# Optimization experiments

Hardware: AMD Instinct MI355X
Metric: run time of the kernel (lower is better)

The kernel has to match this reference:

```python
import jax, jax.numpy as jnp
import numpy as np

B, L, DIM, NH = 32, 512, 256, 4
HD = DIM // NH  # head_size = 64
SCALE = float(np.sqrt(HD))


def setup_inputs() -> dict:
    key = jax.random.key(0)
    k1, k2, k3, k4 = jax.random.split(key, 4)
    x = jax.random.normal(k1, (B, L, DIM), dtype=jnp.float32)
    adj = jax.random.randint(k2, (B, L, L), 0, 16, dtype=jnp.int32)
    w_qkv = jax.random.normal(k3, (3 * DIM, DIM), dtype=jnp.float32) * 0.02
    w_proj = jax.random.normal(k4, (DIM, DIM), dtype=jnp.float32) * 0.02
    return {"x": x, "adj": adj, "w_qkv": w_qkv, "w_proj": w_proj}


def reference(x, adj, w_qkv, w_proj):
    # qkv projection (torch Linear, no bias: y = x @ W.T)
    qkv = x @ w_qkv.T  # [B, L, 3*DIM]
    q, k, v = jnp.split(qkv, 3, axis=-1)
    q = q.reshape(B, L, NH, HD).transpose(0, 2, 1, 3)  # [B, H, L, HD]
    k = k.reshape(B, L, NH, HD).transpose(0, 2, 1, 3)
    v = v.reshape(B, L, NH, HD).transpose(0, 2, 1, 3)

    score = jnp.einsum('bhqd,bhkd->bhqk', q, k) / SCALE  # [B, H, L, L]

    # rel_pos_bias adjacency mask construction
    a = jnp.where((adj > 1) & (adj < 9), 0, adj)
    a = (a != 0).astype(jnp.float32)               # binarized adjacency [B, L, L]
    aT = jnp.swapaxes(a, -1, -2)
    pe = jnp.stack([a, aT, aT @ a, a @ aT], axis=1)  # [B, 4, L, L]
    pe = pe + jnp.eye(L, dtype=jnp.float32)
    pe = pe.astype(jnp.int32)

    score = jnp.where(pe == 0, -jnp.inf, score)
    attn = jax.nn.softmax(score, axis=-1)
    out = jnp.einsum('bhqk,bhkd->bhqd', attn, v)   # [B, H, L, HD]
    out = out.transpose(0, 2, 1, 3).reshape(B, L, DIM)
    return out @ w_proj.T
```

## Files before the change

### kernel.cpp

```cpp
#include <hip/hip_runtime.h>


typedef unsigned long long u64;
typedef unsigned short u16;
typedef short bf16x8 __attribute__((ext_vector_type(8)));
typedef float f32x4 __attribute__((ext_vector_type(4)));

#define MFMA16(a, b, c) __builtin_amdgcn_mfma_f32_16x16x32_bf16((a), (b), (c), 0, 0, 0)

__device__ __forceinline__ unsigned f2bf(float f) {
  unsigned u = __float_as_uint(f);
  return (u + 0x7FFFu + ((u >> 16) & 1u)) >> 16;
}
__device__ __forceinline__ float bf2f(unsigned b) { return __uint_as_float(b << 16); }

__device__ __forceinline__ unsigned cvtpk(float lo, float hi) {
  unsigned r;
  asm("v_cvt_pk_bf16_f32 %0, %1, %2" : "=v"(r) : "v"(lo), "v"(hi));
  return r;
}

__device__ __forceinline__ void gload16(const u16* src, u16* ldsDst) {
  __builtin_amdgcn_global_load_lds(
      (const __attribute__((address_space(1))) void*)src,
      (__attribute__((address_space(3))) void*)ldsDst, 16, 0, 0);
}

__device__ __forceinline__ int swzE(int row, int e) {
  return row * 64 + (e ^ ((row & 7) << 3));
}
__device__ __forceinline__ int swzV(int row, int c) {
  return row * 512 + (c ^ ((row & 7) << 3));
}

#define OFF_XB    ((size_t)0)
#define OFF_WQKV  ((size_t)8388608)
#define OFF_WPA   ((size_t)8781824)
#define OFF_QB    ((size_t)9175040)
#define OFF_KB    ((size_t)17563648)
#define OFF_VTB   ((size_t)25952256)
#define OFF_CTXA  ((size_t)34340864)
#define OFF_ROWR  ((size_t)51118080)
#define OFF_COLR  ((size_t)52166656)
#define OFF_MASK  ((size_t)53215232)

__global__ __launch_bounds__(512) void prep(const float* __restrict__ x, u16* __restrict__ xb,
                                            const float* __restrict__ wqkv, u16* __restrict__ wqkvb,
                                            const float* __restrict__ wp, u16* __restrict__ wpa,
                                            const int* __restrict__ adj, u64* __restrict__ rowraw,
                                            u64* __restrict__ maskA0) {
  int blk = blockIdx.x;
  if (blk < 1072) {
    const float* src = (blk < 1024) ? x : wqkv;
    u16* dst = (blk < 1024) ? xb : wqkvb;
    int bb = (blk < 1024) ? blk : (blk - 1024);
    size_t i = ((size_t)bb * 512 + threadIdx.x) * 8;
    float4 a = *(const float4*)(src + i);
    float4 c = *(const float4*)(src + i + 4);
    uint4 o;
    o.x = f2bf(a.x) | (f2bf(a.y) << 16);
    o.y = f2bf(a.z) | (f2bf(a.w) << 16);
    o.z = f2bf(c.x) | (f2bf(c.y) << 16);
    o.w = f2bf(c.z) | (f2bf(c.w) << 16);
    *(uint4*)(dst + i) = o;
  } else if (blk < 1200) {
    int idx = (blk - 1072) * 512 + threadIdx.x;
    int n = idx >> 8, k = idx & 255;
    float v = wp[idx];
    unsigned hi = f2bf(v);
    unsigned lo = f2bf(v - bf2f(hi));
    size_t base = (size_t)n * 768;
    wpa[base + k]       = (u16)hi;
    wpa[base + 256 + k] = (u16)hi;
    wpa[base + 512 + k] = (u16)lo;
  } else {
    int blk2 = blk - 1200;
    int b = blk2 >> 6, r0 = (blk2 & 63) * 8;
    int wave = threadIdx.x >> 6, lane = threadIdx.x & 63;
    #pragma unroll
    for (int rr = 0; rr < 8; ++rr) {
      int row = r0 + rr;
      int v = adj[((size_t)b * 512 + row) * 512 + wave * 64 + lane];
      u64 bal = __ballot(v == 1 || v >= 9);
      if (lane == 0) {
        size_t o = ((size_t)b * 512 + row) * 8 + wave;
        rowraw[o] = bal;
        maskA0[o] = bal | (((row >> 6) == wave) ? (1ull << (row & 63)) : 0ull);
      }
    }
  }
}

__global__ __launch_bounds__(512) void maskall(const u64* __restrict__ rowraw,
                                               u64* __restrict__ maskA1,
                                               u64* __restrict__ maskA2,
                                               u64* __restrict__ maskA3) {
  __shared__ u64 btr[8 * 512];
  __shared__ u64 cbuf[512 * 8];
  int b = blockIdx.x, tid = threadIdx.x;
  {
    const u64* src = rowraw + (size_t)b * 4096 + (size_t)tid * 8;
    u64 r[8];
    #pragma unroll
    for (int w = 0; w < 8; ++w) r[w] = src[w];
    #pragma unroll
    for (int w = 0; w < 8; ++w) btr[w * 512 + tid] = r[w];
  }
  __syncthreads();
  int w = tid >> 6, lane = tid & 63;
  u64 words[8];
  #pragma unroll
  for (int wd = 0; wd < 8; ++wd) {
    u64 word = btr[w * 512 + wd * 64 + lane];
    u64 mine = 0;
    #pragma unroll 1
    for (int c = 0; c < 64; ++c) {
      u64 bal = __ballot((word >> c) & 1ull);
      if (lane == c) mine = bal;
    }
    words[wd] = mine;
  }
  {
    u64* m1 = maskA1 + (size_t)b * 4096 + (size_t)tid * 8;
    #pragma unroll
    for (int wd = 0; wd < 8; ++wd) cbuf[tid * 8 + wd] = words[wd];
    words[w] |= (1ull << lane);
    #pragma unroll
    for (int wd = 0; wd < 8; ++wd) m1[wd] = words[wd];
  }
  __syncthreads();

  u64 myrow[8], mycol[8];
  #pragma unroll
  for (int w2 = 0; w2 < 8; ++w2) { myrow[w2] = btr[w2 * 512 + tid]; mycol[w2] = cbuf[tid * 8 + w2]; }
  u64 a2[8] = {0, 0, 0, 0, 0, 0, 0, 0}, a3[8] = {0, 0, 0, 0, 0, 0, 0, 0};
  for (int c0 = 0; c0 < 512; c0 += 64) {
    for (int cc = 0; cc < 64; ++cc) {
      int c = c0 + cc;
      u64 p3 = 0ull - ((myrow[c >> 6] >> (c & 63)) & 1ull);
      u64 p2 = 0ull - ((mycol[c >> 6] >> (c & 63)) & 1ull);
      #pragma unroll
      for (int w2 = 0; w2 < 8; ++w2) {
        a3[w2] |= cbuf[c * 8 + w2] & p3;
        a2[w2] |= btr[w2 * 512 + c] & p2;
      }
    }
    u64 f = ~0ull;
    #pragma unroll
    for (int w2 = 0; w2 < 8; ++w2) f &= (a2[w2] & a3[w2]);
    if (__all((int)(f == ~0ull))) break;
  }
  #pragma unroll
  for (int w2 = 0; w2 < 8; ++w2) {
    u64 eye = ((tid >> 6) == w2) ? (1ull << (tid & 63)) : 0ull;
    size_t o = (size_t)b * 4096 + (size_t)tid * 8 + w2;
    maskA2[o] = a2[w2] | eye;
    maskA3[o] = a3[w2] | eye;
  }
}

__global__ __launch_bounds__(256) void gemm_qkv(const u16* __restrict__ A,
                                                const u16* __restrict__ Bw,
                                                u16* __restrict__ o_q, u16* __restrict__ o_k,
                                                u16* __restrict__ o_v) {
  __shared__ u16 As[128 * 64];
  __shared__ u16 Bs[128 * 64];
  const int lin = blockIdx.x;
  const int logical = (lin & 7) * 96 + (lin >> 3);
  const int m0 = (logical / 6) * 128, n0 = (logical % 6) * 128;
  const int tid = threadIdx.x;
  const int lane = tid & 63, wid = tid >> 6;
  const int lg = lane >> 4, lc = lane & 15;
  const int wm = wid >> 1, wn = wid & 1;
  f32x4 acc[4][4] = {};

  const int srow = lane >> 3;
  const int schunk = ((lane & 7) ^ srow) * 8;
  #define STAGE_QKV(ks)                                                        \
    {                                                                          \
      int kk0 = (ks) * 64;                                                     \
      _Pragma("unroll")                                                        \
      for (int j = 0; j < 4; ++j) {                                            \
        int slab = wid * 4 + j;                                                \
        int r = slab * 8 + srow;                                               \
        gload16(A + (size_t)(m0 + r) * 256 + kk0 + schunk, &As[slab * 512]);   \
        gload16(Bw + (size_t)(n0 + r) * 256 + kk0 + schunk, &Bs[slab * 512]);  \
      }                                                                        \
    }

  STAGE_QKV(0);
  for (int ks = 0; ks < 4; ++ks) {
    __syncthreads();
    bf16x8 af[2][4], bf[2][4];
    #pragma unroll
    for (int kk = 0; kk < 2; ++kk)
      #pragma unroll
      for (int mi = 0; mi < 4; ++mi) {
        af[kk][mi] = *(const bf16x8*)&As[swzE(wm * 64 + mi * 16 + lc, kk * 32 + lg * 8)];
        bf[kk][mi] = *(const bf16x8*)&Bs[swzE(wn * 64 + mi * 16 + lc, kk * 32 + lg * 8)];
      }
    __syncthreads();
    if (ks < 3) STAGE_QKV(ks + 1);
    #pragma unroll
    for (int kk = 0; kk < 2; ++kk)
      #pragma unroll
      for (int mi = 0; mi < 4; ++mi)
        #pragma unroll
        for (int ni = 0; ni < 4; ++ni)
          acc[mi][ni] = MFMA16(af[kk][mi], bf[kk][ni], acc[mi][ni]);
  }
  #undef STAGE_QKV

  #pragma unroll
  for (int mi = 0; mi < 4; ++mi) {
    int mbase = m0 + wm * 64 + mi * 16 + lg * 4;
    int bb = mbase >> 9, l = mbase & 511;
    #pragma unroll
    for (int ni = 0; ni < 4; ++ni) {
      int n = n0 + wn * 64 + ni * 16 + lc;
      if (n < 512) {
        u16* dst = (n < 256) ? o_q : o_k;
        int c = n & 255, hh = c >> 6, dd = c & 63;
        size_t base = (((size_t)bb * 4 + hh) * 512 + l) * 64 + dd;
        #pragma unroll
        for (int r = 0; r < 4; ++r) dst[base + (size_t)r * 64] = (u16)f2bf(acc[mi][ni][r]);
      } else {
        int c = n - 512, hh = c >> 6, dd = c & 63;
        ushort4 pk;
        pk.x = (u16)f2bf(acc[mi][ni][0]); pk.y = (u16)f2bf(acc[mi][ni][1]);
        pk.z = (u16)f2bf(acc[mi][ni][2]); pk.w = (u16)f2bf(acc[mi][ni][3]);
        *(ushort4*)&o_v[(((size_t)bb * 4 + hh) * 64 + dd) * 512 + l] = pk;
      }
    }
  }
}

__global__ __launch_bounds__(256) void gemm_out(const u16* __restrict__ A,
                                                const u16* __restrict__ Bw,
                                                float* __restrict__ o_f) {
  __shared__ u16 As[64 * 64];
  __shared__ u16 Bs[128 * 64];
  const int lin = blockIdx.x;
  const int logical = (lin & 7) * 64 + (lin >> 3);
  const int m0 = (logical >> 1) * 64, n0 = (logical & 1) * 128;
  const int tid = threadIdx.x;
  const int lane = tid & 63, wid = tid >> 6;
  const int lg = lane >> 4, lc = lane & 15;
  const int wm = wid >> 1, wn = wid & 1;
  f32x4 acc[2][4] = {};

  const int srow = lane >> 3;
  const int schunk = ((lane & 7) ^ srow) * 8;
  #define STAGE_OUT(ks)                                                        \
    {                                                                          \
      int k0 = (ks) * 64;                                                      \
      int ka0 = (k0 >= 512) ? k0 - 512 : k0;                                   \
      _Pragma("unroll")                                                        \
      for (int j = 0; j < 2; ++j) {                                            \
        int slab = wid * 2 + j;                                                \
        int r = slab * 8 + srow;                                               \
        gload16(A + (size_t)(m0 + r) * 512 + ka0 + schunk, &As[slab * 512]);   \
      }                                                                        \
      _Pragma("unroll")                                                        \
      for (int j = 0; j < 4; ++j) {                                            \
        int slab = wid * 4 + j;                                                \
        int r = slab * 8 + srow;                                               \
        gload16(Bw + (size_t)(n0 + r) * 768 + k0 + schunk, &Bs[slab * 512]);   \
      }                                                                        \
    }

  STAGE_OUT(0);
  for (int ks = 0; ks < 12; ++ks) {
    __syncthreads();
    bf16x8 af[2][2], bf[2][4];
    #pragma unroll
    for (int kk = 0; kk < 2; ++kk) {
      #pragma unroll
      for (int mi = 0; mi < 2; ++mi)
        af[kk][mi] = *(const bf16x8*)&As[swzE(wm * 32 + mi * 16 + lc, kk * 32 + lg * 8)];
      #pragma unroll
      for (int ni = 0; ni < 4; ++ni)
        bf[kk][ni] = *(const bf16x8*)&Bs[swzE(wn * 64 + ni * 16 + lc, kk * 32 + lg * 8)];
    }
    __syncthreads();
    if (ks < 11) STAGE_OUT(ks + 1);
    #pragma unroll
    for (int kk = 0; kk < 2; ++kk)
      #pragma unroll
      for (int mi = 0; mi < 2; ++mi)
        #pragma unroll
        for (int ni = 0; ni < 4; ++ni)
          acc[mi][ni] = MFMA16(af[kk][mi], bf[kk][ni], acc[mi][ni]);
  }
  #undef STAGE_OUT

  #pragma unroll
  for (int mi = 0; mi < 2; ++mi) {
    int mbase = m0 + wm * 32 + mi * 16 + lg * 4;
    #pragma unroll
    for (int ni = 0; ni < 4; ++ni) {
      int n = n0 + wn * 64 + ni * 16 + lc;
      #pragma unroll
      for (int r = 0; r < 4; ++r) o_f[(size_t)(mbase + r) * 256 + n] = acc[mi][ni][r];
    }
  }
}

__device__ __forceinline__ void p_step(const f32x4 sT[4], u64 mw, int lane, u16* PsW,
                                       float& lrun, bf16x8& ap0, bf16x8& ap1) {
  const float SC = 0.125f * 1.4426950408889634f;
  const int lg = lane >> 4, lc = lane & 15;
  float p[4][4];
  float ps = 0.f;
  #pragma unroll
  for (int nf = 0; nf < 4; ++nf)
    #pragma unroll
    for (int r = 0; r < 4; ++r) {
      bool ok = (mw >> (nf * 16 + r)) & 1ull;
      float e = __builtin_amdgcn_exp2f(sT[nf][r] * SC);
      e = ok ? e : 0.f;
      p[nf][r] = e;
      ps += e;
    }
  lrun += ps;

  #pragma unroll
  for (int nf = 0; nf < 4; ++nf) {
    uint2 w2;
    w2.x = cvtpk(p[nf][0], p[nf][1]);
    w2.y = cvtpk(p[nf][2], p[nf][3]);
    *(uint2*)&PsW[swzE(lc, nf * 16 + lg * 4)] = w2;
  }
  ap0 = *(const bf16x8*)&PsW[swzE(lc, lg * 8)];
  ap1 = *(const bf16x8*)&PsW[swzE(lc, lg * 8 + 32)];
}

__global__ __launch_bounds__(512, 1) void attn(const u16* __restrict__ qb, const u16* __restrict__ kb,
                                               const u16* __restrict__ vtb, const u64* __restrict__ maskA,
                                               u16* __restrict__ ctxa) {
  __shared__ u16 Ks[512 * 64];
  __shared__ u16 Vs[64 * 512];
  __shared__ u16 Ps[8][16 * 64];
  const int lin = blockIdx.x;
  const int logical = (lin & 7) * 32 + (lin >> 3);
  const int bh = logical >> 1, half = logical & 1;
  const int b = bh >> 2, h = bh & 3;
  const int tid = threadIdx.x, lane = tid & 63, wid = tid >> 6;
  const int lg = lane >> 4, lc = lane & 15;

  {
    const u16* kgs = kb + (size_t)bh * 512 * 64;
    const u16* vgs = vtb + (size_t)bh * 64 * 512;
    const int srow = lane >> 3;
    const int schunk = ((lane & 7) ^ srow) * 8;
    #pragma unroll
    for (int j = 0; j < 8; ++j) {
      int slab = wid * 8 + j;
      gload16(kgs + (size_t)(slab * 8 + srow) * 64 + schunk, &Ks[slab * 512]);
    }
    #pragma unroll
    for (int j = 0; j < 8; ++j) {
      int vr = wid * 8 + j;
      gload16(vgs + (size_t)vr * 512 + ((lane ^ (vr & 7)) * 8), &Vs[vr * 512]);
    }
  }

  const int qrow0 = half * 256 + wid * 32;
  const u16* qgA = qb + ((size_t)bh * 512 + qrow0 + lc) * 64;
  const u16* qgB = qgA + 16 * 64;
  bf16x8 qA0 = *(const bf16x8*)(qgA + lg * 8);
  bf16x8 qA1 = *(const bf16x8*)(qgA + 32 + lg * 8);
  bf16x8 qB0 = *(const bf16x8*)(qgB + lg * 8);
  bf16x8 qB1 = *(const bf16x8*)(qgB + 32 + lg * 8);

  float lrunA = 0.f, lrunB = 0.f;
  f32x4 accoA[4] = {}, accoB[4] = {};
  const u64* mrowA = maskA + ((size_t)(h * 32 + b) * 512 + qrow0 + lc) * 8;
  const u64* mrowB = mrowA + 16 * 8;
  u16* PsW = Ps[wid];

  u64 mwA = mrowA[0], mwB = mrowB[0];

  __syncthreads();

  for (int kt = 0; kt < 8; ++kt) {
    u64 nmwA = (kt < 7) ? mrowA[kt + 1] : 0ull;
    u64 nmwB = (kt < 7) ? mrowB[kt + 1] : 0ull;

    f32x4 sA[4], sB[4];
    __builtin_amdgcn_s_setprio(1);
    #pragma unroll
    for (int nf = 0; nf < 4; ++nf) {
      bf16x8 ak0 = *(const bf16x8*)&Ks[swzE(kt * 64 + nf * 16 + lc, lg * 8)];
      bf16x8 ak1 = *(const bf16x8*)&Ks[swzE(kt * 64 + nf * 16 + lc, lg * 8 + 32)];
      f32x4 zA = {0.f, 0.f, 0.f, 0.f};
      zA = MFMA16(ak0, qA0, zA);
      zA = MFMA16(ak1, qA1, zA);
      sA[nf] = zA;
      f32x4 zB = {0.f, 0.f, 0.f, 0.f};
      zB = MFMA16(ak0, qB0, zB);
      zB = MFMA16(ak1, qB1, zB);
      sB[nf] = zB;
    }
    __builtin_amdgcn_s_setprio(0);

    bf16x8 apA0, apA1, apB0, apB1;
    p_step(sA, mwA >> (lg * 4), lane, PsW, lrunA, apA0, apA1);
    p_step(sB, mwB >> (lg * 4), lane, PsW, lrunB, apB0, apB1);

    __builtin_amdgcn_s_setprio(1);
    #pragma unroll
    for (int df = 0; df < 4; ++df) {
      bf16x8 bv0 = *(const bf16x8*)&Vs[swzV(df * 16 + lc, kt * 64 + lg * 8)];
      bf16x8 bv1 = *(const bf16x8*)&Vs[swzV(df * 16 + lc, kt * 64 + 32 + lg * 8)];
      accoA[df] = MFMA16(apA0, bv0, accoA[df]);
      accoA[df] = MFMA16(apA1, bv1, accoA[df]);
      accoB[df] = MFMA16(apB0, bv0, accoB[df]);
      accoB[df] = MFMA16(apB1, bv1, accoB[df]);
    }
    __builtin_amdgcn_s_setprio(0);

    mwA = nmwA;
    mwB = nmwB;
  }

  lrunA += __shfl_xor(lrunA, 16);
  lrunA += __shfl_xor(lrunA, 32);
  lrunB += __shfl_xor(lrunB, 16);
  lrunB += __shfl_xor(lrunB, 32);
  float lrA[4], lrB[4];
  #pragma unroll
  for (int r = 0; r < 4; ++r) {
    lrA[r] = 1.0f / __shfl(lrunA, (lane & 48) | (lg * 4 + r));
    lrB[r] = 1.0f / __shfl(lrunB, (lane & 48) | (lg * 4 + r));
  }
  #pragma unroll
  for (int r = 0; r < 4; ++r) {
    int rowq = qrow0 + lg * 4 + r;
    size_t baseA = ((size_t)b * 512 + rowq) * 512;
    size_t baseB = ((size_t)b * 512 + rowq + 16) * 512;
    #pragma unroll
    for (int df = 0; df < 4; ++df) {
      int c = h * 64 + df * 16 + lc;
      float vA = accoA[df][r] * lrA[r];
      unsigned hiA = f2bf(vA);
      ctxa[baseA + c]       = (u16)hiA;
      ctxa[baseA + 256 + c] = (u16)f2bf(vA - bf2f(hiA));
      float vB = accoB[df][r] * lrB[r];
      unsigned hiB = f2bf(vB);
      ctxa[baseB + c]       = (u16)hiB;
      ctxa[baseB + 256 + c] = (u16)f2bf(vB - bf2f(hiB));
    }
  }
}

extern "C" void kernel_launch(void* const* d_in, const int* in_sizes, int n_in,
                              void* d_out, int out_size, void* d_ws, size_t ws_size,
                              hipStream_t stream) {
  const float* x     = (const float*)d_in[0];
  const int*   adj   = (const int*)d_in[1];
  const float* wqkv  = (const float*)d_in[2];
  const float* wproj = (const float*)d_in[3];
  char* ws = (char*)d_ws;
  u16* xb     = (u16*)(ws + OFF_XB);
  u16* wqkvb  = (u16*)(ws + OFF_WQKV);
  u16* wpa    = (u16*)(ws + OFF_WPA);
  u16* qb     = (u16*)(ws + OFF_QB);
  u16* kb     = (u16*)(ws + OFF_KB);
  u16* vtb    = (u16*)(ws + OFF_VTB);
  u16* ctxa   = (u16*)(ws + OFF_CTXA);
  u64* rowraw = (u64*)(ws + OFF_ROWR);
  u64* maskA  = (u64*)(ws + OFF_MASK);
  const size_t MSTRIDE = (size_t)32 * 512 * 8;

  prep<<<dim3(3248), 512, 0, stream>>>(x, xb, wqkv, wqkvb, wproj, wpa, adj, rowraw, maskA);
  maskall<<<dim3(32), 512, 0, stream>>>(rowraw, maskA + MSTRIDE, maskA + 2 * MSTRIDE, maskA + 3 * MSTRIDE);
  gemm_qkv<<<dim3(768), 256, 0, stream>>>(xb, wqkvb, qb, kb, vtb);
  attn<<<dim3(256), 512, 0, stream>>>(qb, kb, vtb, maskA, ctxa);
  gemm_out<<<dim3(512), 256, 0, stream>>>(ctxa, wpa, (float*)d_out);
}
```

Baseline: 104.5 us.

## Split mask kernel into bit transpose and parallel mask products across more blocks

```diff
diff --git a/kernel.cpp b/kernel.cpp
--- a/kernel.cpp
+++ b/kernel.cpp
@@ -91,12 +91,10 @@
   }
 }
 
-__global__ __launch_bounds__(512) void maskall(const u64* __restrict__ rowraw,
-                                               u64* __restrict__ maskA1,
-                                               u64* __restrict__ maskA2,
-                                               u64* __restrict__ maskA3) {
+__global__ __launch_bounds__(512) void transpose_bits(const u64* __restrict__ rowraw,
+                                                      u64* __restrict__ colraw,
+                                                      u64* __restrict__ maskA1) {
   __shared__ u64 btr[8 * 512];
-  __shared__ u64 cbuf[512 * 8];
   int b = blockIdx.x, tid = threadIdx.x;
   {
     const u64* src = rowraw + (size_t)b * 4096 + (size_t)tid * 8;
@@ -120,43 +118,60 @@
     }
     words[wd] = mine;
   }
-  {
-    u64* m1 = maskA1 + (size_t)b * 4096 + (size_t)tid * 8;
-    #pragma unroll
-    for (int wd = 0; wd < 8; ++wd) cbuf[tid * 8 + wd] = words[wd];
-    words[w] |= (1ull << lane);
-    #pragma unroll
-    for (int wd = 0; wd < 8; ++wd) m1[wd] = words[wd];
+  int col = w * 64 + lane;
+  u64* crow = colraw + (size_t)b * 4096 + (size_t)col * 8;
+  u64* mrow = maskA1 + (size_t)b * 4096 + (size_t)col * 8;
+  #pragma unroll
+  for (int wd = 0; wd < 8; ++wd) crow[wd] = words[wd];
+  words[w] |= (1ull << lane);
+  #pragma unroll
+  for (int wd = 0; wd < 8; ++wd) mrow[wd] = words[wd];
+}
+
+__global__ __launch_bounds__(512) void mask23p(const u64* __restrict__ rowraw,
+                                               const u64* __restrict__ colraw,
+                                               u64* __restrict__ maskA2,
+                                               u64* __restrict__ maskA3) {
+  __shared__ u64 rb[4104];
+  __shared__ u64 cb[4104];
+  const int b = blockIdx.x, qc = blockIdx.y, tid = threadIdx.x;
+  for (int i = tid; i < 4096; i += 512) {
+    int li = i + (i >> 9);
+    rb[li] = rowraw[(size_t)b * 4096 + i];
+    cb[li] = colraw[(size_t)b * 4096 + i];
   }
   __syncthreads();
 
-  u64 myrow[8], mycol[8];
-  #pragma unroll
-  for (int w2 = 0; w2 < 8; ++w2) { myrow[w2] = btr[w2 * 512 + tid]; mycol[w2] = cbuf[tid * 8 + w2]; }
+  const int ql = tid >> 3, wg = tid & 7;
+  const int q = qc * 64 + ql;
+  const u64 myrow_w = rb[q * 8 + wg + (q >> 6)];
+  const u64 mycol_w = cb[q * 8 + wg + (q >> 6)];
+
   u64 a2[8] = {0, 0, 0, 0, 0, 0, 0, 0}, a3[8] = {0, 0, 0, 0, 0, 0, 0, 0};
-  for (int c0 = 0; c0 < 512; c0 += 64) {
-    for (int cc = 0; cc < 64; ++cc) {
-      int c = c0 + cc;
-      u64 p3 = 0ull - ((myrow[c >> 6] >> (c & 63)) & 1ull);
-      u64 p2 = 0ull - ((mycol[c >> 6] >> (c & 63)) & 1ull);
-      #pragma unroll
-      for (int w2 = 0; w2 < 8; ++w2) {
-        a3[w2] |= cbuf[c * 8 + w2] & p3;
-        a2[w2] |= btr[w2 * 512 + c] & p2;
-      }
-    }
-    u64 f = ~0ull;
-    #pragma unroll
-    for (int w2 = 0; w2 < 8; ++w2) f &= (a2[w2] & a3[w2]);
-    if (__all((int)(f == ~0ull))) break;
-  }
-  #pragma unroll
-  for (int w2 = 0; w2 < 8; ++w2) {
-    u64 eye = ((tid >> 6) == w2) ? (1ull << (tid & 63)) : 0ull;
-    size_t o = (size_t)b * 4096 + (size_t)tid * 8 + w2;
-    maskA2[o] = a2[w2] | eye;
-    maskA3[o] = a3[w2] | eye;
-  }
+  #pragma unroll 4
+  for (int cc = 0; cc < 64; ++cc) {
+    int base = (wg * 64 + cc) * 8 + wg;
+    u64 p3 = 0ull - ((myrow_w >> cc) & 1ull);
+    u64 p2 = 0ull - ((mycol_w >> cc) & 1ull);
+    #pragma unroll
+    for (int w = 0; w < 8; ++w) {
+      a3[w] |= cb[base + w] & p3;
+      a2[w] |= rb[base + w] & p2;
+    }
+  }
+
+  #pragma unroll
+  for (int off = 1; off < 8; off <<= 1)
+    #pragma unroll
+    for (int w = 0; w < 8; ++w) {
+      a2[w] |= __shfl_xor(a2[w], off);
+      a3[w] |= __shfl_xor(a3[w], off);
+    }
+
+  u64 eye = ((q >> 6) == wg) ? (1ull << (q & 63)) : 0ull;
+  size_t o = (size_t)b * 4096 + (size_t)q * 8 + wg;
+  maskA2[o] = a2[wg] | eye;
+  maskA3[o] = a3[wg] | eye;
 }
 
 __global__ __launch_bounds__(256) void gemm_qkv(const u16* __restrict__ A,
@@ -470,11 +485,13 @@
   u16* vtb    = (u16*)(ws + OFF_VTB);
   u16* ctxa   = (u16*)(ws + OFF_CTXA);
   u64* rowraw = (u64*)(ws + OFF_ROWR);
+  u64* colraw = (u64*)(ws + OFF_COLR);
   u64* maskA  = (u64*)(ws + OFF_MASK);
   const size_t MSTRIDE = (size_t)32 * 512 * 8;
 
   prep<<<dim3(3248), 512, 0, stream>>>(x, xb, wqkv, wqkvb, wproj, wpa, adj, rowraw, maskA);
-  maskall<<<dim3(32), 512, 0, stream>>>(rowraw, maskA + MSTRIDE, maskA + 2 * MSTRIDE, maskA + 3 * MSTRIDE);
+  transpose_bits<<<dim3(32), 512, 0, stream>>>(rowraw, colraw, maskA + MSTRIDE);
+  mask23p<<<dim3(32, 8), 512, 0, stream>>>(rowraw, colraw, maskA + 2 * MSTRIDE, maskA + 3 * MSTRIDE);
   gemm_qkv<<<dim3(768), 256, 0, stream>>>(xb, wqkvb, qb, kb, vtb);
   attn<<<dim3(256), 512, 0, stream>>>(qb, kb, vtb, maskA, ctxa);
   gemm_out<<<dim3(512), 256, 0, stream>>>(ctxa, wpa, (float*)d_out);
```

Result: slower. 114.3 us (+9.4%).

## Split boolean mask product into parallel transpose and per-word intersection kernels

Applied to the files above, without the earlier changes.

```diff
diff --git a/kernel.cpp b/kernel.cpp
--- a/kernel.cpp
+++ b/kernel.cpp
@@ -91,71 +91,54 @@
   }
 }
 
-__global__ __launch_bounds__(512) void maskall(const u64* __restrict__ rowraw,
-                                               u64* __restrict__ maskA1,
-                                               u64* __restrict__ maskA2,
-                                               u64* __restrict__ maskA3) {
-  __shared__ u64 btr[8 * 512];
-  __shared__ u64 cbuf[512 * 8];
-  int b = blockIdx.x, tid = threadIdx.x;
+__global__ __launch_bounds__(512) void transposeW(const u64* __restrict__ rowraw,
+                                                  u64* __restrict__ colraw,
+                                                  u64* __restrict__ maskA1) {
+  const int b = blockIdx.x, wd = blockIdx.y;
+  const int tid = threadIdx.x, w = tid >> 6, t = tid & 63;
+  u64 rw = rowraw[(size_t)b * 4096 + (size_t)(wd * 64 + t) * 8 + w];
+  u64 mine = 0;
+  #pragma unroll 1
+  for (int cbit = 0; cbit < 64; ++cbit) {
+    u64 bal = __ballot((rw >> cbit) & 1ull);
+    if (t == cbit) mine = bal;
+  }
+  int col = w * 64 + t;
+  size_t o = (size_t)b * 4096 + (size_t)col * 8 + wd;
+  colraw[o] = mine;
+  u64 eye = (w == wd) ? (1ull << t) : 0ull;
+  maskA1[o] = mine | eye;
+}
+
+__global__ __launch_bounds__(512) void maskp(const u64* __restrict__ rowraw,
+                                             const u64* __restrict__ colraw,
+                                             u64* __restrict__ maskA2,
+                                             u64* __restrict__ maskA3) {
+  __shared__ u64 rows[512][9];
+  const int b = blockIdx.x, w = blockIdx.y, type = blockIdx.z;
+  const int tid = threadIdx.x, wavid = tid >> 6, lane = tid & 63;
+  const u64* src = type ? rowraw : colraw;
+  u64* dst = type ? maskA3 : maskA2;
   {
-    const u64* src = rowraw + (size_t)b * 4096 + (size_t)tid * 8;
-    u64 r[8];
-    #pragma unroll
-    for (int w = 0; w < 8; ++w) r[w] = src[w];
-    #pragma unroll
-    for (int w = 0; w < 8; ++w) btr[w * 512 + tid] = r[w];
+    const u64* s = src + (size_t)b * 4096 + (size_t)tid * 8;
+    #pragma unroll
+    for (int k = 0; k < 8; ++k) rows[tid][k] = s[k];
   }
   __syncthreads();
-  int w = tid >> 6, lane = tid & 63;
-  u64 words[8];
-  #pragma unroll
-  for (int wd = 0; wd < 8; ++wd) {
-    u64 word = btr[w * 512 + wd * 64 + lane];
-    u64 mine = 0;
-    #pragma unroll 1
-    for (int c = 0; c < 64; ++c) {
-      u64 bal = __ballot((word >> c) & 1ull);
-      if (lane == c) mine = bal;
-    }
-    words[wd] = mine;
-  }
-  {
-    u64* m1 = maskA1 + (size_t)b * 4096 + (size_t)tid * 8;
-    #pragma unroll
-    for (int wd = 0; wd < 8; ++wd) cbuf[tid * 8 + wd] = words[wd];
-    words[w] |= (1ull << lane);
-    #pragma unroll
-    for (int wd = 0; wd < 8; ++wd) m1[wd] = words[wd];
-  }
-  __syncthreads();
-
-  u64 myrow[8], mycol[8];
-  #pragma unroll
-  for (int w2 = 0; w2 < 8; ++w2) { myrow[w2] = btr[w2 * 512 + tid]; mycol[w2] = cbuf[tid * 8 + w2]; }
-  u64 a2[8] = {0, 0, 0, 0, 0, 0, 0, 0}, a3[8] = {0, 0, 0, 0, 0, 0, 0, 0};
-  for (int c0 = 0; c0 < 512; c0 += 64) {
-    for (int cc = 0; cc < 64; ++cc) {
-      int c = c0 + cc;
-      u64 p3 = 0ull - ((myrow[c >> 6] >> (c & 63)) & 1ull);
-      u64 p2 = 0ull - ((mycol[c >> 6] >> (c & 63)) & 1ull);
-      #pragma unroll
-      for (int w2 = 0; w2 < 8; ++w2) {
-        a3[w2] |= cbuf[c * 8 + w2] & p3;
-        a2[w2] |= btr[w2 * 512 + c] & p2;
-      }
-    }
-    u64 f = ~0ull;
-    #pragma unroll
-    for (int w2 = 0; w2 < 8; ++w2) f &= (a2[w2] & a3[w2]);
-    if (__all((int)(f == ~0ull))) break;
-  }
-  #pragma unroll
-  for (int w2 = 0; w2 < 8; ++w2) {
-    u64 eye = ((tid >> 6) == w2) ? (1ull << (tid & 63)) : 0ull;
-    size_t o = (size_t)b * 4096 + (size_t)tid * 8 + w2;
-    maskA2[o] = a2[w2] | eye;
-    maskA3[o] = a3[w2] | eye;
+  u64 jr[8];
+  #pragma unroll
+  for (int k = 0; k < 8; ++k) jr[k] = rows[w * 64 + lane][k];
+  #pragma unroll 4
+  for (int qq = 0; qq < 64; ++qq) {
+    int q = wavid * 64 + qq;
+    u64 x = 0;
+    #pragma unroll
+    for (int k = 0; k < 8; ++k) x |= jr[k] & rows[q][k];
+    u64 word = __ballot(x != 0ull);
+    if (lane == qq) {
+      u64 eye = (wavid == w) ? (1ull << qq) : 0ull;
+      dst[(size_t)b * 4096 + (size_t)q * 8 + w] = word | eye;
+    }
   }
 }
 
@@ -470,11 +453,13 @@
   u16* vtb    = (u16*)(ws + OFF_VTB);
   u16* ctxa   = (u16*)(ws + OFF_CTXA);
   u64* rowraw = (u64*)(ws + OFF_ROWR);
+  u64* colraw = (u64*)(ws + OFF_COLR);
   u64* maskA  = (u64*)(ws + OFF_MASK);
   const size_t MSTRIDE = (size_t)32 * 512 * 8;
 
   prep<<<dim3(3248), 512, 0, stream>>>(x, xb, wqkv, wqkvb, wproj, wpa, adj, rowraw, maskA);
-  maskall<<<dim3(32), 512, 0, stream>>>(rowraw, maskA + MSTRIDE, maskA + 2 * MSTRIDE, maskA + 3 * MSTRIDE);
+  transposeW<<<dim3(32, 8), 512, 0, stream>>>(rowraw, colraw, maskA + MSTRIDE);
+  maskp<<<dim3(32, 8, 2), 512, 0, stream>>>(rowraw, colraw, maskA + 2 * MSTRIDE, maskA + 3 * MSTRIDE);
   gemm_qkv<<<dim3(768), 256, 0, stream>>>(xb, wqkvb, qb, kb, vtb);
   attn<<<dim3(256), 512, 0, stream>>>(qb, kb, vtb, maskA, ctxa);
   gemm_out<<<dim3(512), 256, 0, stream>>>(ctxa, wpa, (float*)d_out);
```

New measurement: 85.99 us (median of 2 runs). 1.22x faster.
